# Optimization experiments

Hardware: AMD Instinct MI355X
Metric: run time of the kernel (lower is better)

The kernel has to match this reference:

```python
import jax, jax.numpy as jnp
import numpy as np

# per-item cutpoint counts (from np.unique(item_positions, return_counts=True))
NUM_CUTS = np.array([4, 5, 6, 7] * 4)  # 16 items
N_ITEMS = len(NUM_CUTS)
MAX_CP = int(NUM_CUTS.max())  # 7
CP = jnp.asarray(NUM_CUTS)  # [I]
CUT_MASK = jnp.arange(MAX_CP)[None, :] < CP[:, None]  # [I, MAX_CP] valid cutpoints
EPS = 1e-8

B, D_IN, H1, H2 = 65536, 512, 1024, 512


def setup_inputs() -> dict:
    key = jax.random.key(0)
    ks = jax.random.split(key, 10)
    x = jax.random.normal(ks[0], (B, D_IN), dtype=jnp.float32)
    data = jax.random.randint(ks[1], (B, N_ITEMS), 0, 4, dtype=jnp.int64 if jax.config.jax_enable_x64 else jnp.int32)
    W1 = jax.random.normal(ks[2], (D_IN, H1), dtype=jnp.float32) / np.sqrt(D_IN)
    b1 = jnp.zeros((H1,), jnp.float32)
    W2 = jax.random.normal(ks[3], (H1, H2), dtype=jnp.float32) / np.sqrt(H1)
    b2 = jnp.zeros((H2,), jnp.float32)
    Wf = jax.random.normal(ks[4], (H2, N_ITEMS), dtype=jnp.float32) / np.sqrt(H2)
    bf = jnp.zeros((N_ITEMS,), jnp.float32)
    # ragged per-item cutpoint heads padded to MAX_CP (masked in reference)
    Wk = jax.random.normal(ks[5], (N_ITEMS, H2, MAX_CP), dtype=jnp.float32) / np.sqrt(H2)
    bk = jnp.zeros((N_ITEMS, MAX_CP), jnp.float32)
    return {"x": x, "data": data, "W1": W1, "b1": b1, "W2": W2, "b2": b2,
            "Wf": Wf, "bf": bf, "Wk": Wk, "bk": bk}


def reference(x, data, W1, b1, W2, b2, Wf, bf, Wk, bk):
    # trunk MLP: Linear -> ReLU, twice
    h = jax.nn.relu(x @ W1 + b1)
    h = jax.nn.relu(h @ W2 + b2)  # [B, H2]
    f_x = h @ Wf + bf  # [B, I]
    # batched ragged per-item cutpoint heads (padded GEMM + mask)
    cut = jnp.einsum('bh,ihc->bic', h, Wk) + bk  # [B, I, MAX_CP]
    e = jnp.where(CUT_MASK[None], jnp.clip(jnp.exp(cut), EPS, None), 0.0)
    cum = jnp.cumsum(e, axis=-1)  # monotone cutpoints; pads contribute 0
    cum_probs = jnp.clip(jax.nn.sigmoid(cum - f_x[:, :, None]), EPS, 1.0 - EPS)
    # category probs: [cum0, diffs..., 1 - cum_last], ragged lengths cp_i + 1
    diff = jnp.concatenate([cum_probs[..., :1], cum_probs[..., 1:] - cum_probs[..., :-1]], axis=-1)
    last_cum = cum_probs[:, jnp.arange(N_ITEMS), CP - 1]  # [B, I]
    diff_pad = jnp.pad(diff, ((0, 0), (0, 0), (0, 1)))  # [B, I, MAX_CP+1]
    cat = jnp.arange(MAX_CP + 1)[None, None, :]
    probs = jnp.where(cat < CP[None, :, None], diff_pad,
                      jnp.where(cat == CP[None, :, None], (1.0 - last_cum)[:, :, None], 1.0))
    probs = jnp.clip(probs, EPS, 1.0 - EPS)  # [B, I, MAX_CP+1]
    # NLL: gather observed category per (respondent, item)
    gathered = jnp.take_along_axis(probs, data[:, :, None].astype(jnp.int32), axis=2)[..., 0]
    rec_loss = -jnp.log(gathered).mean(axis=0).sum()
    return rec_loss, probs
```

## Files before the change

### kernel.cpp

```cpp
#include <hip/hip_runtime.h>
#include <cmath>

#define EPSV 1e-8f

typedef __bf16 bf16_t;
typedef __bf16 bf16x8 __attribute__((ext_vector_type(8)));
typedef __bf16 bf16x4 __attribute__((ext_vector_type(4)));
typedef float f32x4 __attribute__((ext_vector_type(4)));

__device__ __forceinline__ void gload16(const void* g, void* l) {
    __builtin_amdgcn_global_load_lds(
        (const __attribute__((address_space(1))) void*)g,
        (__attribute__((address_space(3))) void*)l, 16, 0, 0);
}

__device__ __forceinline__ void qmap(int q, int& row, int& u) {
    int prow = q >> 3;
    int v = (q & 7) ^ (prow & 7);
    row = (prow << 1) | (v >> 2);
    u = v & 3;
}
__device__ __forceinline__ int lds_elem(int row, int u) {
    int prow = row >> 1;
    int v = ((row & 1) << 2) | u;
    return prow * 64 + ((v ^ (prow & 7)) << 3);
}

template<bool RELU>
__global__ __launch_bounds__(512, 2) void gemm256(
    const bf16_t* __restrict__ A, const bf16_t* __restrict__ BT,
    const float* __restrict__ bias, bf16_t* __restrict__ C,
    int N, int K, int nbx)
{
    __shared__ bf16_t smem[4][2][8192];

    const int t    = threadIdx.x;
    const int lane = t & 63;
    const int w    = t >> 6;
    const int wr   = w >> 2;
    const int wc   = w & 3;
    const int r16  = lane & 15;
    const int u16  = lane >> 4;

    const int nwg = gridDim.x;
    int bid = blockIdx.x;
    int swz = ((nwg & 7) == 0) ? ((bid & 7) * (nwg >> 3) + (bid >> 3)) : bid;
    const int bx = swz % nbx, by = swz / nbx;
    const int m0 = by << 8, n0 = bx << 8;

    int r0, u0, r1, u1;
    qmap(t, r0, u0);
    qmap(t + 512, r1, u1);
    const bf16_t* gA0 = A  + (size_t)(m0 + r0) * K + (u0 << 3);
    const bf16_t* gA1 = A  + (size_t)(m0 + r1) * K + (u1 << 3);
    const bf16_t* gB0 = BT + (size_t)(n0 + r0) * K + (u0 << 3);
    const bf16_t* gB1 = BT + (size_t)(n0 + r1) * K + (u1 << 3);

    int aoff[8], boff[4];
#pragma unroll
    for (int i = 0; i < 8; ++i) aoff[i] = lds_elem((wr << 7) + (i << 4) + r16, u16);
#pragma unroll
    for (int j = 0; j < 4; ++j) boff[j] = lds_elem((wc << 6) + (j << 4) + r16, u16);

    f32x4 acc[8][4];
#pragma unroll
    for (int i = 0; i < 8; ++i)
#pragma unroll
        for (int j = 0; j < 4; ++j) acc[i][j] = (f32x4){0.f, 0.f, 0.f, 0.f};

    const int NT = K >> 5;

#pragma unroll
    for (int p = 0; p < 3; ++p) {
        if (p < NT) {
            const int ko = p << 5;
            bf16_t* s0 = &smem[p][0][w << 9];
            bf16_t* s1 = &smem[p][1][w << 9];
            gload16(gA0 + ko, s0);
            gload16(gA1 + ko, s0 + 4096);
            gload16(gB0 + ko, s1);
            gload16(gB1 + ko, s1 + 4096);
        }
    }
    if (NT > 2)      asm volatile("s_waitcnt vmcnt(8)" ::: "memory");
    else if (NT > 1) asm volatile("s_waitcnt vmcnt(4)" ::: "memory");
    else             asm volatile("s_waitcnt vmcnt(0)" ::: "memory");
    __builtin_amdgcn_s_barrier();

    for (int kt = 0; kt < NT; ++kt) {
        const int b  = kt & 3;
        const int bs = (kt + 3) & 3;
        const int ko3 = (kt + 3) << 5;
        const bool st = (kt + 3) < NT;
        const bf16_t* sA = &smem[b][0][0];
        const bf16_t* sB = &smem[b][1][0];

        bf16x8 bfr[4], af[4];
#pragma unroll
        for (int j = 0; j < 4; ++j) bfr[j] = *(const bf16x8*)(sB + boff[j]);
#pragma unroll
        for (int i = 0; i < 4; ++i) af[i] = *(const bf16x8*)(sA + aoff[i]);
        if (st) {
            bf16_t* d = &smem[bs][0][w << 9];
            gload16(gA0 + ko3, d);
            gload16(gA1 + ko3, d + 4096);
        }
        __builtin_amdgcn_s_barrier();
        asm volatile("s_waitcnt lgkmcnt(0)" ::: "memory");
        __builtin_amdgcn_sched_barrier(0);
        __builtin_amdgcn_s_setprio(1);
#pragma unroll
        for (int i = 0; i < 4; ++i)
#pragma unroll
            for (int j = 0; j < 4; ++j)
                acc[i][j] = __builtin_amdgcn_mfma_f32_16x16x32_bf16(bfr[j], af[i], acc[i][j], 0, 0, 0);
        __builtin_amdgcn_s_setprio(0);
        __builtin_amdgcn_sched_barrier(0);
        __builtin_amdgcn_s_barrier();

        bf16x8 af2[4];
#pragma unroll
        for (int i = 0; i < 4; ++i) af2[i] = *(const bf16x8*)(sA + aoff[4 + i]);
        if (st) {
            bf16_t* d = &smem[bs][1][w << 9];
            gload16(gB0 + ko3, d);
            gload16(gB1 + ko3, d + 4096);
        }
        __builtin_amdgcn_s_barrier();
        asm volatile("s_waitcnt lgkmcnt(0)" ::: "memory");
        __builtin_amdgcn_sched_barrier(0);
        __builtin_amdgcn_s_setprio(1);
#pragma unroll
        for (int i = 0; i < 4; ++i)
#pragma unroll
            for (int j = 0; j < 4; ++j)
                acc[4 + i][j] = __builtin_amdgcn_mfma_f32_16x16x32_bf16(bfr[j], af2[i], acc[4 + i][j], 0, 0, 0);
        __builtin_amdgcn_s_setprio(0);
        __builtin_amdgcn_sched_barrier(0);
        if (st)                  asm volatile("s_waitcnt vmcnt(8)" ::: "memory");
        else if (kt + 2 < NT)    asm volatile("s_waitcnt vmcnt(4)" ::: "memory");
        else if (kt + 1 < NT)    asm volatile("s_waitcnt vmcnt(0)" ::: "memory");
        __builtin_amdgcn_s_barrier();
    }

    char* eb = (char*)&smem[0][0][0];
    const int mBb = (wr << 7) + r16;
    const int nBb = (wc << 6) + (u16 << 2);
#pragma unroll
    for (int i = 0; i < 8; ++i) {
        const int m = mBb + (i << 4);
        const int xm = (m & 3) << 4;
#pragma unroll
        for (int j = 0; j < 4; ++j) {
            const int nl = nBb + (j << 4);
            f32x4 bv = *(const f32x4*)(bias + n0 + nl);
            bf16x4 pk;
#pragma unroll
            for (int r = 0; r < 4; ++r) {
                float v = acc[i][j][r] + bv[r];
                if (RELU) v = fmaxf(v, 0.f);
                pk[r] = (bf16_t)v;
            }
            *(bf16x4*)(eb + m * 512 + ((nl << 1) ^ xm)) = pk;
        }
    }
    __syncthreads();
    const int c  = t & 31;
    const int rr = t >> 5;
#pragma unroll
    for (int rp = 0; rp < 16; ++rp) {
        const int m = (rp << 4) + rr;
        bf16x8 v = *(const bf16x8*)(eb + m * 512 + ((c << 4) ^ ((m & 3) << 4)));
        *(bf16x8*)(C + (size_t)(m0 + m) * N + n0 + (c << 3)) = v;
    }
}

#define BM 128
#define BN 128
#define BK 32

template<bool RELU, typename OutT>
__global__ __launch_bounds__(256) void gemm_bf16(
    const bf16_t* __restrict__ A, const bf16_t* __restrict__ BT,
    const float* __restrict__ bias, OutT* __restrict__ C,
    int N, int K)
{
    __shared__ __align__(16) bf16_t As[BM * BK];
    __shared__ __align__(16) bf16_t Bs[BN * BK];

    const int t    = threadIdx.x;
    const int lane = t & 63;
    const int w    = t >> 6;
    const int wm   = (w >> 1) << 6;
    const int wn   = (w & 1) << 6;
    const int m0   = blockIdx.y * BM;
    const int n0   = blockIdx.x * BN;

    const int srow  = t >> 2;
    const int skoff = (t & 3) << 3;

    const bf16_t* Ap = A  + (size_t)(m0 + srow) * K + skoff;
    const bf16_t* Bp = BT + (size_t)(n0 + srow) * K + skoff;
    const size_t rstep = (size_t)64 * K;

    bf16_t* lA0 = As + ((w << 6)      ) * 8;
    bf16_t* lA1 = As + ((w << 6) + 256) * 8;
    bf16_t* lB0 = Bs + ((w << 6)      ) * 8;
    bf16_t* lB1 = Bs + ((w << 6) + 256) * 8;

    f32x4 acc[4][4];
#pragma unroll
    for (int i = 0; i < 4; ++i)
#pragma unroll
        for (int j = 0; j < 4; ++j) acc[i][j] = (f32x4){0.f, 0.f, 0.f, 0.f};

    const int r16  = lane & 15;
    const int kblk = (lane >> 4) << 3;

    for (int k0 = 0; k0 < K; k0 += BK) {
        __syncthreads();
        gload16(Ap + k0,         lA0);
        gload16(Ap + rstep + k0, lA1);
        gload16(Bp + k0,         lB0);
        gload16(Bp + rstep + k0, lB1);
        __syncthreads();

        bf16x8 af[4], bfr[4];
#pragma unroll
        for (int i = 0; i < 4; ++i) {
            af[i]  = *(const bf16x8*)&As[(wm + (i << 4) + r16) * BK + kblk];
            bfr[i] = *(const bf16x8*)&Bs[(wn + (i << 4) + r16) * BK + kblk];
        }
#pragma unroll
        for (int i = 0; i < 4; ++i)
#pragma unroll
            for (int j = 0; j < 4; ++j)
                acc[i][j] = __builtin_amdgcn_mfma_f32_16x16x32_bf16(af[i], bfr[j], acc[i][j], 0, 0, 0);
    }

#pragma unroll
    for (int j = 0; j < 4; ++j) {
        const int col = n0 + wn + (j << 4) + r16;
        const float bv = bias[col];
#pragma unroll
        for (int i = 0; i < 4; ++i) {
            const int rb = m0 + wm + (i << 4) + ((lane >> 4) << 2);
#pragma unroll
            for (int r = 0; r < 4; ++r) {
                float v = acc[i][j][r] + bv;
                if (RELU) v = fmaxf(v, 0.f);
                C[(size_t)(rb + r) * N + col] = (OutT)v;
            }
        }
    }
}

__global__ __launch_bounds__(256) void convert_x(
    const float* __restrict__ in, bf16_t* __restrict__ out, int n8)
{
    int i = blockIdx.x * 256 + threadIdx.x;
    if (i >= n8) return;
    const float4* p = (const float4*)in;
    float4 a = p[2 * i], b = p[2 * i + 1];
    bf16x8 v;
    v[0] = (bf16_t)a.x; v[1] = (bf16_t)a.y; v[2] = (bf16_t)a.z; v[3] = (bf16_t)a.w;
    v[4] = (bf16_t)b.x; v[5] = (bf16_t)b.y; v[6] = (bf16_t)b.z; v[7] = (bf16_t)b.w;
    ((bf16x8*)out)[i] = v;
}

__global__ __launch_bounds__(256) void transpose_w(
    const float* __restrict__ in, bf16_t* __restrict__ out,
    int kshift, int N, int total)
{
    int idx = blockIdx.x * 256 + threadIdx.x;
    if (idx >= total) return;
    int n = idx >> kshift;
    int k = idx & ((1 << kshift) - 1);
    out[idx] = (bf16_t)in[(size_t)k * N + n];
}

__global__ __launch_bounds__(256) void pack_head(
    const float* __restrict__ Wf, const float* __restrict__ bfv,
    const float* __restrict__ Wk, const float* __restrict__ bk,
    bf16_t* __restrict__ WhT, float* __restrict__ bhead)
{
    int idx = blockIdx.x * 256 + threadIdx.x;
    int n = idx >> 9;
    int k = idx & 511;
    float v;
    if (n < 16) {
        v = Wf[k * 16 + n];
    } else {
        int m = n - 16;
        int i = m / 7, c = m % 7;
        v = Wk[(size_t)i * 3584 + (size_t)k * 7 + c];
    }
    WhT[idx] = (bf16_t)v;
    if (idx < 128) bhead[idx] = (idx < 16) ? bfv[idx] : bk[idx - 16];
}

__global__ __launch_bounds__(256) void head_epilogue(
    const float* __restrict__ hd, const int* __restrict__ data,
    float* __restrict__ probs_out, float* __restrict__ partials,
    int row0)
{
    const int t    = threadIdx.x;
    const int lrow = (blockIdx.x << 4) + (t >> 4);
    const int item = t & 15;
    const size_t grow = (size_t)row0 + lrow;
    const float* h = hd + (size_t)lrow * 128;

    const float f  = h[item];
    const int   cp = 4 + (item & 3);

    float cumP[7];
    float cum = 0.f;
#pragma unroll
    for (int c = 0; c < 7; ++c) {
        if (c < cp) {
            float e = fmaxf(expf(h[16 + item * 7 + c]), EPSV);
            cum += e;
            float s = 1.f / (1.f + expf(f - cum));
            cumP[c] = fminf(fmaxf(s, EPSV), 1.f - EPSV);
        } else {
            cumP[c] = 0.f;
        }
    }

    float probs[8];
#pragma unroll
    for (int k = 0; k < 8; ++k) {
        float v;
        if (k < cp) {
            v = (k == 0) ? cumP[0] : (cumP[k] - cumP[k - 1]);
        } else if (k == cp) {
            v = 1.f - cumP[cp - 1];
        } else {
            v = 1.f;
        }
        probs[k] = fminf(fmaxf(v, EPSV), 1.f - EPSV);
    }

    float* dst = probs_out + (grow * 16 + item) * 8;
#pragma unroll
    for (int k = 0; k < 8; ++k) dst[k] = probs[k];

    int d = data[grow * 16 + item];
    float g = probs[0];
#pragma unroll
    for (int k = 1; k < 8; ++k) g = (d == k) ? probs[k] : g;
    float loss = -logf(g);

    __shared__ float red[256];
    red[t] = loss;
    __syncthreads();
#pragma unroll
    for (int s2 = 128; s2 > 0; s2 >>= 1) {
        if (t < s2) red[t] += red[t + s2];
        __syncthreads();
    }
    if (t == 0) partials[(row0 >> 4) + blockIdx.x] = red[0];
}

__global__ __launch_bounds__(256) void reduce_loss(
    const float* __restrict__ partials, int n, float* __restrict__ out, float scale)
{
    __shared__ float red[256];
    float s = 0.f;
    for (int i = threadIdx.x; i < n; i += 256) s += partials[i];
    red[threadIdx.x] = s;
    __syncthreads();
    for (int k = 128; k > 0; k >>= 1) {
        if (threadIdx.x < k) red[threadIdx.x] += red[threadIdx.x + k];
        __syncthreads();
    }
    if (threadIdx.x == 0) out[0] = red[0] * scale;
}

extern "C" void kernel_launch(void* const* d_in, const int* in_sizes, int n_in,
                              void* d_out, int out_size, void* d_ws, size_t ws_size,
                              hipStream_t stream)
{
    const float* x   = (const float*)d_in[0];
    const int*   dat = (const int*)d_in[1];
    const float* W1  = (const float*)d_in[2];
    const float* b1  = (const float*)d_in[3];
    const float* W2  = (const float*)d_in[4];
    const float* b2  = (const float*)d_in[5];
    const float* Wf  = (const float*)d_in[6];
    const float* bfv = (const float*)d_in[7];
    const float* Wk  = (const float*)d_in[8];
    const float* bk  = (const float*)d_in[9];
    float* out = (float*)d_out;

    const int B = 65536, DIN = 512, H1 = 1024, H2 = 512;

    char* cur = (char*)d_ws;
    auto carve = [&](size_t bytes) {
        char* p = cur;
        cur += (bytes + 255) & ~(size_t)255;
        return p;
    };
    float*  partials = (float*)carve(4096 * 4);
    float*  bhead    = (float*)carve(512);
    bf16_t* W1T      = (bf16_t*)carve((size_t)H1 * DIN * 2);
    bf16_t* W2T      = (bf16_t*)carve((size_t)H2 * H1 * 2);
    bf16_t* WhT      = (bf16_t*)carve((size_t)128 * H2 * 2);

    size_t used = (size_t)(cur - (char*)d_ws);
    size_t avail = (ws_size > used + 1024) ? (ws_size - used - 1024) : 0;
    int SLICE = 2048;
    const int cands[6] = {65536, 32768, 16384, 8192, 4096, 2048};
    for (int ci = 0; ci < 6; ++ci) {
        if ((size_t)cands[ci] * 4608 <= avail) { SLICE = cands[ci]; break; }
    }
    bf16_t* xb = (bf16_t*)carve((size_t)SLICE * DIN * 2);
    bf16_t* h1 = (bf16_t*)carve((size_t)SLICE * H1 * 2);
    bf16_t* h2 = (bf16_t*)carve((size_t)SLICE * H2 * 2);
    float*  hd = (float*)carve((size_t)SLICE * 128 * 4);

    transpose_w<<<(H1 * DIN + 255) / 256, 256, 0, stream>>>(W1, W1T, 9,  H1, H1 * DIN);
    transpose_w<<<(H2 * H1 + 255) / 256, 256, 0, stream>>>(W2, W2T, 10, H2, H2 * H1);
    pack_head<<<256, 256, 0, stream>>>(Wf, bfv, Wk, bk, WhT, bhead);

    for (int r0 = 0; r0 < B; r0 += SLICE) {
        convert_x<<<SLICE / 4, 256, 0, stream>>>(x + (size_t)r0 * DIN, xb, SLICE * DIN / 8);
        gemm256<true><<<(SLICE / 256) * (H1 / 256), 512, 0, stream>>>(xb, W1T, b1, h1, H1, DIN, H1 / 256);
        gemm256<true><<<(SLICE / 256) * (H2 / 256), 512, 0, stream>>>(h1, W2T, b2, h2, H2, H1, H2 / 256);
        gemm_bf16<false, float><<<dim3(1, SLICE / 128), 256, 0, stream>>>(h2, WhT, bhead, hd, 128, H2);
        head_epilogue<<<SLICE / 16, 256, 0, stream>>>(hd, dat, out + 1, partials, r0);
    }
    reduce_loss<<<1, 256, 0, stream>>>(partials, B / 16, out, 1.0f / B);
}
```

Before: 261.4 us.

## Merge split half-tile MFMA phases into one phase per k-tile

Restructures the GEMM main loop so each k-tile takes one barrier at the top of the iteration. All eight A fragments and four B fragments are read from LDS up front, all four async global-to-LDS prefetches are issued together, and then 32 MFMAs run back to back. The previous schedule split each tile into two halves with several barriers and explicit lgkmcnt waits; removing them is meant to cut synchronisation stalls. In exchange it needs more live VGPRs for the eight A fragments, which could hurt occupancy, and it leaves LDS-read waits to the compiler.

```diff
diff --git a/kernel.cpp b/kernel.cpp
--- a/kernel.cpp
+++ b/kernel.cpp
@@ -85,9 +85,10 @@
     if (NT > 2)      asm volatile("s_waitcnt vmcnt(8)" ::: "memory");
     else if (NT > 1) asm volatile("s_waitcnt vmcnt(4)" ::: "memory");
     else             asm volatile("s_waitcnt vmcnt(0)" ::: "memory");
-    __builtin_amdgcn_s_barrier();
 
     for (int kt = 0; kt < NT; ++kt) {
+        __builtin_amdgcn_s_barrier();
+        __builtin_amdgcn_sched_barrier(0);
         const int b  = kt & 3;
         const int bs = (kt + 3) & 3;
         const int ko3 = (kt + 3) << 5;
@@ -95,53 +96,34 @@
         const bf16_t* sA = &smem[b][0][0];
         const bf16_t* sB = &smem[b][1][0];
 
-        bf16x8 bfr[4], af[4];
+        bf16x8 bfr[4], af[8];
 #pragma unroll
         for (int j = 0; j < 4; ++j) bfr[j] = *(const bf16x8*)(sB + boff[j]);
 #pragma unroll
-        for (int i = 0; i < 4; ++i) af[i] = *(const bf16x8*)(sA + aoff[i]);
+        for (int i = 0; i < 8; ++i) af[i] = *(const bf16x8*)(sA + aoff[i]);
         if (st) {
-            bf16_t* d = &smem[bs][0][w << 9];
-            gload16(gA0 + ko3, d);
-            gload16(gA1 + ko3, d + 4096);
-        }
-        __builtin_amdgcn_s_barrier();
-        asm volatile("s_waitcnt lgkmcnt(0)" ::: "memory");
-        __builtin_amdgcn_sched_barrier(0);
+            bf16_t* d0 = &smem[bs][0][w << 9];
+            bf16_t* d1 = &smem[bs][1][w << 9];
+            gload16(gA0 + ko3, d0);
+            gload16(gA1 + ko3, d0 + 4096);
+            gload16(gB0 + ko3, d1);
+            gload16(gB1 + ko3, d1 + 4096);
+        }
         __builtin_amdgcn_s_setprio(1);
 #pragma unroll
-        for (int i = 0; i < 4; ++i)
+        for (int i = 0; i < 8; ++i)
 #pragma unroll
             for (int j = 0; j < 4; ++j)
                 acc[i][j] = __builtin_amdgcn_mfma_f32_16x16x32_bf16(bfr[j], af[i], acc[i][j], 0, 0, 0);
         __builtin_amdgcn_s_setprio(0);
-        __builtin_amdgcn_sched_barrier(0);
-        __builtin_amdgcn_s_barrier();
-
-        bf16x8 af2[4];
-#pragma unroll
-        for (int i = 0; i < 4; ++i) af2[i] = *(const bf16x8*)(sA + aoff[4 + i]);
-        if (st) {
-            bf16_t* d = &smem[bs][1][w << 9];
-            gload16(gB0 + ko3, d);
-            gload16(gB1 + ko3, d + 4096);
-        }
-        __builtin_amdgcn_s_barrier();
-        asm volatile("s_waitcnt lgkmcnt(0)" ::: "memory");
-        __builtin_amdgcn_sched_barrier(0);
-        __builtin_amdgcn_s_setprio(1);
-#pragma unroll
-        for (int i = 0; i < 4; ++i)
-#pragma unroll
-            for (int j = 0; j < 4; ++j)
-                acc[4 + i][j] = __builtin_amdgcn_mfma_f32_16x16x32_bf16(bfr[j], af2[i], acc[4 + i][j], 0, 0, 0);
-        __builtin_amdgcn_s_setprio(0);
-        __builtin_amdgcn_sched_barrier(0);
         if (st)                  asm volatile("s_waitcnt vmcnt(8)" ::: "memory");
         else if (kt + 2 < NT)    asm volatile("s_waitcnt vmcnt(4)" ::: "memory");
         else if (kt + 1 < NT)    asm volatile("s_waitcnt vmcnt(0)" ::: "memory");
-        __builtin_amdgcn_s_barrier();
-    }
+    }
+
+    asm volatile("s_waitcnt lgkmcnt(0)" ::: "memory");
+    __builtin_amdgcn_s_barrier();
+    __builtin_amdgcn_sched_barrier(0);
 
     char* eb = (char*)&smem[0][0][0];
     const int mBb = (wr << 7) + r16;
```

After: 262.2 us. About the same (+0.3%).

## Restructure 256x256 GEMM main loop to process two K-slices per iteration

Applied to the files above, without the earlier changes.

The K loop of the 256-tile GEMM now steps 64 per iteration instead of 32. It uses a ping-pong pair of double K-slice LDS buffers in place of a 4-deep ring of single slices. Prefetch of the next slices is interleaved with the four MFMA phases, and vmcnt waits are simplified to fixed counts. This cuts loop overhead and the conditional wait logic per iteration, with LDS usage unchanged. The new scheme assumes K is a multiple of 64 with at least two iterations, and it changes the effective prefetch distance.

```diff
diff --git a/kernel.cpp b/kernel.cpp
--- a/kernel.cpp
+++ b/kernel.cpp
@@ -32,7 +32,7 @@
     const float* __restrict__ bias, bf16_t* __restrict__ C,
     int N, int K, int nbx)
 {
-    __shared__ bf16_t smem[4][2][8192];
+    __shared__ bf16_t sm[2][2][2][8192];
 
     const int t    = threadIdx.x;
     const int lane = t & 63;
@@ -56,6 +56,11 @@
     const bf16_t* gB0 = BT + (size_t)(n0 + r0) * K + (u0 << 3);
     const bf16_t* gB1 = BT + (size_t)(n0 + r1) * K + (u1 << 3);
 
+    auto STAGE = [&](const bf16_t* g0, const bf16_t* g1, bf16_t* sl, int koff) {
+        gload16(g0 + koff, sl + (w << 9));
+        gload16(g1 + koff, sl + 4096 + (w << 9));
+    };
+
     int aoff[8], boff[4];
 #pragma unroll
     for (int i = 0; i < 8; ++i) aoff[i] = lds_elem((wr << 7) + (i << 4) + r16, u16);
@@ -68,43 +73,36 @@
 #pragma unroll
         for (int j = 0; j < 4; ++j) acc[i][j] = (f32x4){0.f, 0.f, 0.f, 0.f};
 
-    const int NT = K >> 5;
-
-#pragma unroll
-    for (int p = 0; p < 3; ++p) {
-        if (p < NT) {
-            const int ko = p << 5;
-            bf16_t* s0 = &smem[p][0][w << 9];
-            bf16_t* s1 = &smem[p][1][w << 9];
-            gload16(gA0 + ko, s0);
-            gload16(gA1 + ko, s0 + 4096);
-            gload16(gB0 + ko, s1);
-            gload16(gB1 + ko, s1 + 4096);
-        }
-    }
-    if (NT > 2)      asm volatile("s_waitcnt vmcnt(8)" ::: "memory");
-    else if (NT > 1) asm volatile("s_waitcnt vmcnt(4)" ::: "memory");
-    else             asm volatile("s_waitcnt vmcnt(0)" ::: "memory");
+    const int NT = K >> 6;
+
+    STAGE(gA0, gA1, &sm[0][0][0][0], 0);
+    STAGE(gB0, gB1, &sm[0][1][0][0], 0);
+    STAGE(gA0, gA1, &sm[0][0][1][0], 32);
+    STAGE(gB0, gB1, &sm[0][1][1][0], 32);
+    STAGE(gA0, gA1, &sm[1][0][0][0], 64);
+    STAGE(gB0, gB1, &sm[1][1][0][0], 64);
+    asm volatile("s_waitcnt vmcnt(8)" ::: "memory");
     __builtin_amdgcn_s_barrier();
 
     for (int kt = 0; kt < NT; ++kt) {
-        const int b  = kt & 3;
-        const int bs = (kt + 3) & 3;
-        const int ko3 = (kt + 3) << 5;
-        const bool st = (kt + 3) < NT;
-        const bf16_t* sA = &smem[b][0][0];
-        const bf16_t* sB = &smem[b][1][0];
-
-        bf16x8 bfr[4], af[4];
-#pragma unroll
-        for (int j = 0; j < 4; ++j) bfr[j] = *(const bf16x8*)(sB + boff[j]);
-#pragma unroll
-        for (int i = 0; i < 4; ++i) af[i] = *(const bf16x8*)(sA + aoff[i]);
-        if (st) {
-            bf16_t* d = &smem[bs][0][w << 9];
-            gload16(gA0 + ko3, d);
-            gload16(gA1 + ko3, d + 4096);
-        }
+        const int c  = kt & 1;
+        const int c1 = c ^ 1;
+        const bool s12 = (kt + 1) < NT;
+        const bool s34 = (kt + 2) < NT;
+        const int k12 = ((kt + 1) << 6) + 32;
+        const int k34 = (kt + 2) << 6;
+        const bf16_t* sA0 = &sm[c][0][0][0];
+        const bf16_t* sA1 = &sm[c][0][1][0];
+        const bf16_t* sB0 = &sm[c][1][0][0];
+        const bf16_t* sB1 = &sm[c][1][1][0];
+
+        bf16x8 af[4], bfr[4];
+
+#pragma unroll
+        for (int j = 0; j < 4; ++j) bfr[j] = *(const bf16x8*)(sB0 + boff[j]);
+#pragma unroll
+        for (int i = 0; i < 4; ++i) af[i] = *(const bf16x8*)(sA0 + aoff[i]);
+        if (s12) STAGE(gA0, gA1, &sm[c1][0][1][0], k12);
         __builtin_amdgcn_s_barrier();
         asm volatile("s_waitcnt lgkmcnt(0)" ::: "memory");
         __builtin_amdgcn_sched_barrier(0);
@@ -118,14 +116,11 @@
         __builtin_amdgcn_sched_barrier(0);
         __builtin_amdgcn_s_barrier();
 
-        bf16x8 af2[4];
-#pragma unroll
-        for (int i = 0; i < 4; ++i) af2[i] = *(const bf16x8*)(sA + aoff[4 + i]);
-        if (st) {
-            bf16_t* d = &smem[bs][1][w << 9];
-            gload16(gB0 + ko3, d);
-            gload16(gB1 + ko3, d + 4096);
-        }
+#pragma unroll
+        for (int i = 0; i < 4; ++i) af[i] = *(const bf16x8*)(sA0 + aoff[4 + i]);
+        if (s12) STAGE(gB0, gB1, &sm[c1][1][1][0], k12);
+        if (s12) asm volatile("s_waitcnt vmcnt(8)" ::: "memory");
+        else     asm volatile("s_waitcnt vmcnt(0)" ::: "memory");
         __builtin_amdgcn_s_barrier();
         asm volatile("s_waitcnt lgkmcnt(0)" ::: "memory");
         __builtin_amdgcn_sched_barrier(0);
@@ -134,16 +129,51 @@
         for (int i = 0; i < 4; ++i)
 #pragma unroll
             for (int j = 0; j < 4; ++j)
-                acc[4 + i][j] = __builtin_amdgcn_mfma_f32_16x16x32_bf16(bfr[j], af2[i], acc[4 + i][j], 0, 0, 0);
+                acc[4 + i][j] = __builtin_amdgcn_mfma_f32_16x16x32_bf16(bfr[j], af[i], acc[4 + i][j], 0, 0, 0);
         __builtin_amdgcn_s_setprio(0);
         __builtin_amdgcn_sched_barrier(0);
-        if (st)                  asm volatile("s_waitcnt vmcnt(8)" ::: "memory");
-        else if (kt + 2 < NT)    asm volatile("s_waitcnt vmcnt(4)" ::: "memory");
-        else if (kt + 1 < NT)    asm volatile("s_waitcnt vmcnt(0)" ::: "memory");
-        __builtin_amdgcn_s_barrier();
-    }
-
-    char* eb = (char*)&smem[0][0][0];
+        __builtin_amdgcn_s_barrier();
+
+#pragma unroll
+        for (int j = 0; j < 4; ++j) bfr[j] = *(const bf16x8*)(sB1 + boff[j]);
+#pragma unroll
+        for (int i = 0; i < 4; ++i) af[i] = *(const bf16x8*)(sA1 + aoff[i]);
+        if (s34) STAGE(gA0, gA1, &sm[c][0][0][0], k34);
+        __builtin_amdgcn_s_barrier();
+        asm volatile("s_waitcnt lgkmcnt(0)" ::: "memory");
+        __builtin_amdgcn_sched_barrier(0);
+        __builtin_amdgcn_s_setprio(1);
+#pragma unroll
+        for (int i = 0; i < 4; ++i)
+#pragma unroll
+            for (int j = 0; j < 4; ++j)
+                acc[i][j] = __builtin_amdgcn_mfma_f32_16x16x32_bf16(bfr[j], af[i], acc[i][j], 0, 0, 0);
+        __builtin_amdgcn_s_setprio(0);
+        __builtin_amdgcn_sched_barrier(0);
+        __builtin_amdgcn_s_barrier();
+
+#pragma unroll
+        for (int i = 0; i < 4; ++i) af[i] = *(const bf16x8*)(sA1 + aoff[4 + i]);
+        if (s34) STAGE(gB0, gB1, &sm[c][1][0][0], k34);
+        if (s34)      asm volatile("s_waitcnt vmcnt(8)" ::: "memory");
+        else if (s12) asm volatile("s_waitcnt vmcnt(4)" ::: "memory");
+        __builtin_amdgcn_s_barrier();
+        asm volatile("s_waitcnt lgkmcnt(0)" ::: "memory");
+        __builtin_amdgcn_sched_barrier(0);
+        __builtin_amdgcn_s_setprio(1);
+#pragma unroll
+        for (int i = 0; i < 4; ++i)
+#pragma unroll
+            for (int j = 0; j < 4; ++j)
+                acc[4 + i][j] = __builtin_amdgcn_mfma_f32_16x16x32_bf16(bfr[j], af[i], acc[4 + i][j], 0, 0, 0);
+        __builtin_amdgcn_s_setprio(0);
+        __builtin_amdgcn_sched_barrier(0);
+        __builtin_amdgcn_s_barrier();
+    }
+
+    __syncthreads();
+
+    char* eb = (char*)&sm[0][0][0][0];
     const int mBb = (wr << 7) + r16;
     const int nBb = (wc << 6) + (u16 << 2);
 #pragma unroll
@@ -165,13 +195,13 @@
         }
     }
     __syncthreads();
-    const int c  = t & 31;
+    const int cc = t & 31;
     const int rr = t >> 5;
 #pragma unroll
     for (int rp = 0; rp < 16; ++rp) {
         const int m = (rp << 4) + rr;
-        bf16x8 v = *(const bf16x8*)(eb + m * 512 + ((c << 4) ^ ((m & 3) << 4)));
-        *(bf16x8*)(C + (size_t)(m0 + m) * N + n0 + (c << 3)) = v;
+        bf16x8 v = *(const bf16x8*)(eb + m * 512 + ((cc << 4) ^ ((m & 3) << 4)));
+        *(bf16x8*)(C + (size_t)(m0 + m) * N + n0 + (cc << 3)) = v;
     }
 }
 
```

Result: no change. 261.1 us (-0.1%).
